# Kernel tuning notes

Measured on AMD Instinct MI355X. Metric: run time of the kernel, lower is better.

## Reference

```python
import jax, jax.numpy as jnp
import numpy as np

NUM_CLASS = 1000
DIMS = 2048
NUM_HEADS = 8
HEAD = DIMS // NUM_HEADS  # 256
ALPHA = 0.999
N = 16384


def setup_inputs() -> dict:
    key = jax.random.key(0)
    k1, k2, k3 = jax.random.split(key, 3)
    x = jax.random.normal(k1, (N, DIMS), dtype=jnp.float32)
    labels = jax.random.randint(k2, (N,), 0, NUM_CLASS)
    centers = jax.random.normal(k3, (NUM_CLASS, NUM_HEADS, HEAD), dtype=jnp.float32)
    return {"x": x, "labels": labels, "centers": centers}


def reference(x, labels, centers):
    # gather per-sample centers: [N, H, hd]
    c = centers[labels]
    xh = x.reshape(-1, NUM_HEADS, HEAD)  # [N, H, hd]
    # per-head MSE, sum over heads, mean over batch
    loss = jnp.mean(jnp.square(xh - c), axis=-1).sum(axis=-1).mean()
    new_centers = centers.at[labels].set(ALPHA * c + (1.0 - ALPHA) * xh)
    return loss, new_centers
```

## Files before the change

kernel.cpp:

```cpp
#include <hip/hip_runtime.h>

#define NUM_CLASS 1000
#define DIMS 2048
#define NBATCH 16384
#define ALPHA 0.999f
#define LOSS_SCALE (1.0f / (16384.0f * 256.0f))

#define BLOCK 256
#define NBLOCKS 4096
#define ROWS_PER_BLOCK (NBATCH / NBLOCKS)

typedef float vfloat4 __attribute__((ext_vector_type(4)));

__global__ __launch_bounds__(BLOCK) void fused_kernel(
    const float* __restrict__ x,
    const int* __restrict__ labels,
    const float* __restrict__ centers,
    float* __restrict__ out_loss,
    float* __restrict__ newc) {
    __shared__ float smf[4];
    __shared__ int smi[4];
    const int tid  = threadIdx.x;
    const int lane = tid & 63;
    const int wid  = tid >> 6;
    const int b    = blockIdx.x;

    float acc = 0.0f;
    const int row0 = b * ROWS_PER_BLOCK;
    #pragma unroll
    for (int r = 0; r < ROWS_PER_BLOCK; ++r) {
        const int row   = row0 + r;
        const int label = labels[row];
        const vfloat4* xr = reinterpret_cast<const vfloat4*>(x + (size_t)row * DIMS);
        const vfloat4* cr = reinterpret_cast<const vfloat4*>(centers + (size_t)label * DIMS);
        #pragma unroll
        for (int j = 0; j < DIMS / 4 / BLOCK; ++j) {
            const int e = j * BLOCK + tid;
            vfloat4 xv = __builtin_nontemporal_load(xr + e);
            vfloat4 cv = cr[e];
            vfloat4 d = xv - cv;
            acc += d.x * d.x + d.y * d.y + d.z * d.z + d.w * d.w;
        }
    }
    #pragma unroll
    for (int off = 32; off > 0; off >>= 1)
        acc += __shfl_down(acc, off, 64);
    if (lane == 0) smf[wid] = acc;
    __syncthreads();
    if (tid == 0) {
        float v = (smf[0] + smf[1]) + (smf[2] + smf[3]);
        atomicAdd(out_loss, v * LOSS_SCALE);
    }

    if (b < NUM_CLASS) {
        int best = -1;
        for (int i = tid; i < NBATCH; i += BLOCK) {
            if (labels[i] == b) best = i;
        }
        #pragma unroll
        for (int off = 32; off > 0; off >>= 1) {
            int o = __shfl_down(best, off, 64);
            best = best > o ? best : o;
        }
        if (lane == 0) smi[wid] = best;
        __syncthreads();
        if (tid == 0) {
            int v01 = smi[0] > smi[1] ? smi[0] : smi[1];
            int v23 = smi[2] > smi[3] ? smi[2] : smi[3];
            smi[0] = v01 > v23 ? v01 : v23;
        }
        __syncthreads();
        const int li = smi[0];

        const vfloat4* crow = reinterpret_cast<const vfloat4*>(centers + (size_t)b * DIMS);
        float* orow = newc + (size_t)b * DIMS;
        if (li >= 0) {
            const vfloat4* xrow = reinterpret_cast<const vfloat4*>(x + (size_t)li * DIMS);
            #pragma unroll
            for (int j = 0; j < DIMS / 4 / BLOCK; ++j) {
                const int e = j * BLOCK + tid;
                vfloat4 c4 = crow[e];
                vfloat4 x4 = xrow[e];
                float* o = orow + (size_t)e * 4;
                __builtin_nontemporal_store(ALPHA * c4.x + (1.0f - ALPHA) * x4.x, o + 0);
                __builtin_nontemporal_store(ALPHA * c4.y + (1.0f - ALPHA) * x4.y, o + 1);
                __builtin_nontemporal_store(ALPHA * c4.z + (1.0f - ALPHA) * x4.z, o + 2);
                __builtin_nontemporal_store(ALPHA * c4.w + (1.0f - ALPHA) * x4.w, o + 3);
            }
        } else {
            #pragma unroll
            for (int j = 0; j < DIMS / 4 / BLOCK; ++j) {
                const int e = j * BLOCK + tid;
                vfloat4 c4 = crow[e];
                float* o = orow + (size_t)e * 4;
                __builtin_nontemporal_store(c4.x, o + 0);
                __builtin_nontemporal_store(c4.y, o + 1);
                __builtin_nontemporal_store(c4.z, o + 2);
                __builtin_nontemporal_store(c4.w, o + 3);
            }
        }
    }
}

extern "C" void kernel_launch(void* const* d_in, const int* in_sizes, int n_in,
                              void* d_out, int out_size, void* d_ws, size_t ws_size,
                              hipStream_t stream) {
    const float* x       = (const float*)d_in[0];
    const int*   labels  = (const int*)d_in[1];
    const float* centers = (const float*)d_in[2];

    float* out_loss = (float*)d_out;
    float* out_newc = (float*)d_out + 1;

    (void)hipMemsetAsync(out_loss, 0, sizeof(float), stream);
    fused_kernel<<<NBLOCKS, BLOCK, 0, stream>>>(x, labels, centers,
                                                out_loss, out_newc);
}
```

Before: 234.0 us.

## Split fused kernel and replace per-class label scan with atomicMax last-index

Computes the last occurrence index for each class with atomicMax into a workspace array during the loss pass, instead of having each of the first 1000 blocks scan all labels. The center EMA update moves to a separate kernel that reads that index. The x loads also drop the nontemporal hint. This removes the redundant label scans but adds an extra memset, a second kernel launch and global atomics.

Result: faster. 222.1 us (-5.1%).

```diff
diff --git a/kernel.cpp b/kernel.cpp
--- a/kernel.cpp
+++ b/kernel.cpp
@@ -12,21 +12,24 @@
 
 typedef float vfloat4 __attribute__((ext_vector_type(4)));
 
-__global__ __launch_bounds__(BLOCK) void fused_kernel(
+__global__ __launch_bounds__(BLOCK) void loss_kernel(
     const float* __restrict__ x,
     const int* __restrict__ labels,
     const float* __restrict__ centers,
     float* __restrict__ out_loss,
-    float* __restrict__ newc) {
+    int* __restrict__ last) {
     __shared__ float smf[4];
-    __shared__ int smi[4];
     const int tid  = threadIdx.x;
     const int lane = tid & 63;
     const int wid  = tid >> 6;
-    const int b    = blockIdx.x;
+    const int row0 = blockIdx.x * ROWS_PER_BLOCK;
+
+    if (tid < ROWS_PER_BLOCK) {
+        const int row = row0 + tid;
+        atomicMax(&last[labels[row]], row);
+    }
 
     float acc = 0.0f;
-    const int row0 = b * ROWS_PER_BLOCK;
     #pragma unroll
     for (int r = 0; r < ROWS_PER_BLOCK; ++r) {
         const int row   = row0 + r;
@@ -36,7 +39,7 @@
         #pragma unroll
         for (int j = 0; j < DIMS / 4 / BLOCK; ++j) {
             const int e = j * BLOCK + tid;
-            vfloat4 xv = __builtin_nontemporal_load(xr + e);
+            vfloat4 xv = xr[e];
             vfloat4 cv = cr[e];
             vfloat4 d = xv - cv;
             acc += d.x * d.x + d.y * d.y + d.z * d.z + d.w * d.w;
@@ -51,53 +54,42 @@
         float v = (smf[0] + smf[1]) + (smf[2] + smf[3]);
         atomicAdd(out_loss, v * LOSS_SCALE);
     }
+}
 
-    if (b < NUM_CLASS) {
-        int best = -1;
-        for (int i = tid; i < NBATCH; i += BLOCK) {
-            if (labels[i] == b) best = i;
+__global__ __launch_bounds__(BLOCK) void update_kernel(
+    const float* __restrict__ x,
+    const float* __restrict__ centers,
+    const int* __restrict__ last,
+    float* __restrict__ newc) {
+    const int b   = blockIdx.x;
+    const int tid = threadIdx.x;
+    const int li  = last[b];
+
+    const vfloat4* crow = reinterpret_cast<const vfloat4*>(centers + (size_t)b * DIMS);
+    float* orow = newc + (size_t)b * DIMS;
+    if (li >= 0) {
+        const vfloat4* xrow = reinterpret_cast<const vfloat4*>(x + (size_t)li * DIMS);
+        #pragma unroll
+        for (int j = 0; j < DIMS / 4 / BLOCK; ++j) {
+            const int e = j * BLOCK + tid;
+            vfloat4 c4 = crow[e];
+            vfloat4 x4 = xrow[e];
+            float* o = orow + (size_t)e * 4;
+            __builtin_nontemporal_store(ALPHA * c4.x + (1.0f - ALPHA) * x4.x, o + 0);
+            __builtin_nontemporal_store(ALPHA * c4.y + (1.0f - ALPHA) * x4.y, o + 1);
+            __builtin_nontemporal_store(ALPHA * c4.z + (1.0f - ALPHA) * x4.z, o + 2);
+            __builtin_nontemporal_store(ALPHA * c4.w + (1.0f - ALPHA) * x4.w, o + 3);
         }
+    } else {
         #pragma unroll
-        for (int off = 32; off > 0; off >>= 1) {
-            int o = __shfl_down(best, off, 64);
-            best = best > o ? best : o;
-        }
-        if (lane == 0) smi[wid] = best;
-        __syncthreads();
-        if (tid == 0) {
-            int v01 = smi[0] > smi[1] ? smi[0] : smi[1];
-            int v23 = smi[2] > smi[3] ? smi[2] : smi[3];
-            smi[0] = v01 > v23 ? v01 : v23;
-        }
-        __syncthreads();
-        const int li = smi[0];
-
-        const vfloat4* crow = reinterpret_cast<const vfloat4*>(centers + (size_t)b * DIMS);
-        float* orow = newc + (size_t)b * DIMS;
-        if (li >= 0) {
-            const vfloat4* xrow = reinterpret_cast<const vfloat4*>(x + (size_t)li * DIMS);
-            #pragma unroll
-            for (int j = 0; j < DIMS / 4 / BLOCK; ++j) {
-                const int e = j * BLOCK + tid;
-                vfloat4 c4 = crow[e];
-                vfloat4 x4 = xrow[e];
-                float* o = orow + (size_t)e * 4;
-                __builtin_nontemporal_store(ALPHA * c4.x + (1.0f - ALPHA) * x4.x, o + 0);
-                __builtin_nontemporal_store(ALPHA * c4.y + (1.0f - ALPHA) * x4.y, o + 1);
-                __builtin_nontemporal_store(ALPHA * c4.z + (1.0f - ALPHA) * x4.z, o + 2);
-                __builtin_nontemporal_store(ALPHA * c4.w + (1.0f - ALPHA) * x4.w, o + 3);
-            }
-        } else {
-            #pragma unroll
-            for (int j = 0; j < DIMS / 4 / BLOCK; ++j) {
-                const int e = j * BLOCK + tid;
-                vfloat4 c4 = crow[e];
-                float* o = orow + (size_t)e * 4;
-                __builtin_nontemporal_store(c4.x, o + 0);
-                __builtin_nontemporal_store(c4.y, o + 1);
-                __builtin_nontemporal_store(c4.z, o + 2);
-                __builtin_nontemporal_store(c4.w, o + 3);
-            }
+        for (int j = 0; j < DIMS / 4 / BLOCK; ++j) {
+            const int e = j * BLOCK + tid;
+            vfloat4 c4 = crow[e];
+            float* o = orow + (size_t)e * 4;
+            __builtin_nontemporal_store(c4.x, o + 0);
+            __builtin_nontemporal_store(c4.y, o + 1);
+            __builtin_nontemporal_store(c4.z, o + 2);
+            __builtin_nontemporal_store(c4.w, o + 3);
         }
     }
 }
@@ -111,8 +103,11 @@
 
     float* out_loss = (float*)d_out;
     float* out_newc = (float*)d_out + 1;
+    int*   last     = (int*)d_ws;
 
+    (void)hipMemsetAsync(last, 0xFF, NUM_CLASS * sizeof(int), stream);
     (void)hipMemsetAsync(out_loss, 0, sizeof(float), stream);
-    fused_kernel<<<NBLOCKS, BLOCK, 0, stream>>>(x, labels, centers,
-                                                out_loss, out_newc);
+
+    loss_kernel<<<NBLOCKS, BLOCK, 0, stream>>>(x, labels, centers, out_loss, last);
+    update_kernel<<<NUM_CLASS, BLOCK, 0, stream>>>(x, centers, last, out_newc);
 }
```
